# Optimization experiments

Hardware: AMD Instinct MI355X
Metric: run time of the kernel (lower is better)

The kernel has to match this reference:

```python
import jax, jax.numpy as jnp
import numpy as np

B, T, C = 8, 1024, 768
H = 12
HS = C // H  # 64


def setup_inputs() -> dict:
    key = jax.random.key(0)
    ks = jax.random.split(key, 6)
    s = C ** -0.5
    x = jax.random.normal(ks[0], (B, T, C), dtype=jnp.float32)
    Wq = jax.random.normal(ks[1], (H, C, HS), dtype=jnp.float32) * s
    Wk = jax.random.normal(ks[2], (H, C, HS), dtype=jnp.float32) * s
    Wv = jax.random.normal(ks[3], (H, C, HS), dtype=jnp.float32) * s
    Wproj = jax.random.normal(ks[4], (C, C), dtype=jnp.float32) * s
    bproj = jax.random.normal(ks[5], (C,), dtype=jnp.float32) * 0.01
    return {"x": x, "Wq": Wq, "Wk": Wk, "Wv": Wv, "Wproj": Wproj, "bproj": bproj}


def reference(x, Wq, Wk, Wv, Wproj, bproj):
    # per-head projections (equivalent to stacked per-head nn.Linear, bias=False)
    q = jnp.einsum('btc,hcd->bhtd', x, Wq)
    k = jnp.einsum('btc,hcd->bhtd', x, Wk)
    v = jnp.einsum('btc,hcd->bhtd', x, Wv)
    scale = HS ** -0.5
    scores = jnp.einsum('bhtd,bhsd->bhts', q, k) * scale  # [B,H,T,T]
    causal = jnp.tril(jnp.ones((T, T), dtype=bool))
    scores = jnp.where(causal, scores, -jnp.inf)
    weights = jax.nn.softmax(scores, axis=-1)
    out = jnp.einsum('bhts,bhsd->bhtd', weights, v)  # [B,H,T,HS]
    out = out.transpose(0, 2, 1, 3).reshape(B, T, C)  # concat heads
    # output projection (dropout is identity in eval mode)
    return out @ Wproj.T + bproj
```

## Files before the change

### kernel.cpp

```cpp
#include <hip/hip_runtime.h>
#include <hip/hip_bf16.h>


typedef short bf16x8 __attribute__((ext_vector_type(8)));
typedef float f32x4 __attribute__((ext_vector_type(4)));

static __device__ __forceinline__ unsigned short f2bf(float f) {
  unsigned int u = __float_as_uint(f);
  u += 0x7fffu + ((u >> 16) & 1u);
  return (unsigned short)(u >> 16);
}

static __device__ __forceinline__ unsigned int pk2bf(float a, float b) {
  union { __hip_bfloat162 h; unsigned int u; } c;
  c.h = __float22bfloat162_rn(make_float2(a, b));
  return c.u;
}

static __device__ __forceinline__ void gl_lds16(const void* g, void* l) {
  __builtin_amdgcn_global_load_lds(
      (const __attribute__((address_space(1))) unsigned int*)g,
      (__attribute__((address_space(3))) unsigned int*)l, 16, 0, 0);
}

__global__ __launch_bounds__(256) void k_prep(
    const float* __restrict__ x, const float* __restrict__ Wproj,
    const float* __restrict__ Wq, const float* __restrict__ Wk,
    const float* __restrict__ Wv,
    unsigned short* __restrict__ xb, unsigned short* __restrict__ wp,
    unsigned short* __restrict__ wt) {
  __shared__ float tb[64][65];
  const int bx = blockIdx.x;
  const int tid = threadIdx.x;
  if (bx < 6720) {
    const float* src = (bx < 6144) ? x : Wproj;
    unsigned short* dst = (bx < 6144) ? xb : wp;
    int i = (bx < 6144 ? bx : bx - 6144) * 256 + tid;
    float4 f = ((const float4*)src)[i];
    uint2 o;
    o.x = pk2bf(f.x, f.y);
    o.y = pk2bf(f.z, f.w);
    ((uint2*)dst)[i] = o;
    return;
  }
  const int idx = bx - 6720;
  const int c0 = (idx % 12) * 64;
  const int hq = idx / 12;
  const int qi = hq / 12, h = hq % 12;
  const float* W = (qi == 0) ? Wq : ((qi == 1) ? Wk : Wv);
  {
    int rowb = tid >> 4;
    int col4 = (tid & 15) * 4;
#pragma unroll
    for (int it = 0; it < 4; ++it) {
      int c = it * 16 + rowb;
      float4 f = *(const float4*)(W + (h * 768 + c0 + c) * 64 + col4);
      tb[c][col4] = f.x; tb[c][col4 + 1] = f.y; tb[c][col4 + 2] = f.z; tb[c][col4 + 3] = f.w;
    }
  }
  __syncthreads();
#pragma unroll
  for (int it = 0; it < 2; ++it) {
    int slot = it * 256 + tid;
    int d = slot >> 3, cg = (slot & 7) * 8;
    union { unsigned int u[4]; uint4 v; } o;
#pragma unroll
    for (int j = 0; j < 4; ++j)
      o.u[j] = pk2bf(tb[cg + 2 * j][d], tb[cg + 2 * j + 1][d]);
    *(uint4*)(wt + (qi * 768 + h * 64 + d) * 768 + c0 + cg) = o.v;
  }
}

__global__ __launch_bounds__(256) void k_gemm_qkv(
    const unsigned short* __restrict__ xb,
    const unsigned short* __restrict__ wt,
    unsigned short* __restrict__ qkv,
    unsigned short* __restrict__ vt) {
  __shared__ unsigned short As[128 * 32];
  __shared__ unsigned short Bs[128 * 32];
  const int tid = threadIdx.x;
  const int w = tid >> 6, lane = tid & 63, quad = lane >> 4, lr = lane & 15;
  const int wm = w >> 1, wn = w & 1;
  const int m0 = blockIdx.x * 128, n0 = blockIdx.y * 128;

  f32x4 acc[4][4] = {};

  const int srow = w * 16 + (lane >> 2);
  const int su = (lane & 3) ^ ((srow >> 1) & 3);
  const int scol = su * 8;
  const unsigned short* ga0 = xb + (m0 + srow) * 768 + scol;
  const unsigned short* ga1 = ga0 + 64 * 768;
  const unsigned short* gb0 = wt + (n0 + srow) * 768 + scol;
  const unsigned short* gb1 = gb0 + 64 * 768;
  unsigned short* la0 = &As[(w * 16) * 32];
  unsigned short* la1 = la0 + 64 * 32;
  unsigned short* lb0 = &Bs[(w * 16) * 32];
  unsigned short* lb1 = lb0 + 64 * 32;

  const int fu = quad ^ ((lr >> 1) & 3);

  for (int k0 = 0; k0 < 768; k0 += 32) {
    gl_lds16(ga0 + k0, la0);
    gl_lds16(ga1 + k0, la1);
    gl_lds16(gb0 + k0, lb0);
    gl_lds16(gb1 + k0, lb1);
    __syncthreads();
    bf16x8 af[4], bfr[4];
#pragma unroll
    for (int i = 0; i < 4; ++i)
      af[i] = *(const bf16x8*)(&As[(wm * 64 + i * 16 + lr) * 32 + fu * 8]);
#pragma unroll
    for (int j = 0; j < 4; ++j)
      bfr[j] = *(const bf16x8*)(&Bs[(wn * 64 + j * 16 + lr) * 32 + fu * 8]);
#pragma unroll
    for (int j = 0; j < 4; ++j)
#pragma unroll
      for (int i = 0; i < 4; ++i)
        acc[j][i] = __builtin_amdgcn_mfma_f32_16x16x32_bf16(bfr[j], af[i], acc[j][i], 0, 0, 0);
    __syncthreads();
  }

  const int b = m0 >> 10, t0 = m0 & 1023;
  if (n0 < 1536) {
    const int qi = n0 / 768;
    const int rr0 = n0 - qi * 768;
#pragma unroll
    for (int j = 0; j < 4; ++j) {
      int nn = rr0 + wn * 64 + j * 16 + quad * 4;
      int h = nn >> 6, d0 = nn & 63;
      unsigned short* hb = qkv + (size_t)((qi * 8 + b) * 12 + h) * 65536 + d0;
#pragma unroll
      for (int i = 0; i < 4; ++i) {
        int t = t0 + wm * 64 + i * 16 + lr;
        uint2 o;
        o.x = pk2bf(acc[j][i][0], acc[j][i][1]);
        o.y = pk2bf(acc[j][i][2], acc[j][i][3]);
        *(uint2*)(hb + (size_t)t * 64) = o;
      }
    }
  } else {
    const int rr0 = n0 - 1536;
#pragma unroll
    for (int j = 0; j < 4; ++j) {
      int nn = rr0 + wn * 64 + j * 16 + quad * 4;
      int h = nn >> 6, d0 = nn & 63;
      unsigned short* vrow = vt + (size_t)((b * 12 + h) * 64 + d0) * 1024;
#pragma unroll
      for (int i = 0; i < 4; ++i) {
        int t = t0 + wm * 64 + i * 16 + lr;
#pragma unroll
        for (int r = 0; r < 4; ++r)
          vrow[(size_t)r * 1024 + t] = f2bf(acc[j][i][r]);
      }
    }
  }
}

__global__ __launch_bounds__(256) void k_attn(
    const unsigned short* __restrict__ qkv,
    const unsigned short* __restrict__ Vtg,
    unsigned short* __restrict__ attn) {
  __shared__ unsigned short Kbuf[2][64 * 64];
  __shared__ unsigned short Vbuf[2][64 * 64];
  __shared__ unsigned short Pbuf[4][32 * 68];
  const int tid = threadIdx.x;
  const int w = tid >> 6, lane = tid & 63, quad = lane >> 4, lr = lane & 15;
  const int hb = blockIdx.x;
  const int qb = 7 - (int)blockIdx.y;
  const int h = hb % 12, b = hb / 12;
  const int HT = 65536;
  const unsigned short* Q  = qkv + (b * 12 + h) * HT;
  const unsigned short* K  = qkv + (96 + b * 12 + h) * HT;
  const unsigned short* Vt = Vtg + (b * 12 + h) * HT;

  bf16x8 aq[2][2];
#pragma unroll
  for (int i = 0; i < 2; ++i)
#pragma unroll
    for (int hf = 0; hf < 2; ++hf)
      aq[i][hf] = *(const bf16x8*)(Q + (qb * 128 + w * 32 + i * 16 + lr) * 64 + hf * 32 + quad * 8);

  f32x4 accO[2][4] = {};
  float lsum[2][4] = {};

  const int nc = 2 * qb + 2;
  const float c1 = 0.125f * 1.4426950408889634f;
  const float c0 = -4.0f * 1.4426950408889634f;

  auto stage = [&](int bi, int sc) {
#pragma unroll
    for (int j = 0; j < 2; ++j) {
      int row = w * 16 + j * 8 + (lane >> 3);
      int c8 = (lane & 7) ^ (row & 7);
      gl_lds16(K + (sc * 64 + row) * 64 + c8 * 8, &Kbuf[bi][(w * 16 + j * 8) * 64]);
      gl_lds16(Vt + row * 1024 + sc * 64 + c8 * 8, &Vbuf[bi][(w * 16 + j * 8) * 64]);
    }
  };

  stage(0, 0);
  for (int sc = 0; sc < nc; ++sc) {
    __syncthreads();
    if (sc + 1 < nc) stage((sc + 1) & 1, sc + 1);
    const unsigned short* Kl = Kbuf[sc & 1];
    const unsigned short* Vl = Vbuf[sc & 1];

    f32x4 accS[2][4];
#pragma unroll
    for (int i = 0; i < 2; ++i)
#pragma unroll
      for (int nt = 0; nt < 4; ++nt) {
        f32x4 z = {};
#pragma unroll
        for (int hf = 0; hf < 2; ++hf) {
          int s = nt * 16 + lr;
          bf16x8 kb = *(const bf16x8*)(Kl + (s * 8 + ((4 * hf + quad) ^ (s & 7))) * 8);
          z = __builtin_amdgcn_mfma_f32_16x16x32_bf16(aq[i][hf], kb, z, 0, 0, 0);
        }
        accS[i][nt] = z;
      }

#pragma unroll
    for (int i = 0; i < 2; ++i) {
      const int base_i = qb * 128 + w * 32 + i * 16;
      const bool needmask = (sc * 64 + 63 > base_i);
#pragma unroll
      for (int r = 0; r < 4; ++r) {
        int tg = base_i + quad * 4 + r;
        unsigned short* prow = &Pbuf[w][(i * 16 + quad * 4 + r) * 68 + lr];
        float p[4];
#pragma unroll
        for (int nt = 0; nt < 4; ++nt) {
          float e = __builtin_amdgcn_exp2f(fmaf(accS[i][nt][r], c1, c0));
          if (needmask && (sc * 64 + nt * 16 + lr > tg)) e = 0.f;
          lsum[i][r] += e;
          p[nt] = e;
        }
        unsigned int u01 = pk2bf(p[0], p[1]);
        unsigned int u23 = pk2bf(p[2], p[3]);
        prow[0]  = (unsigned short)(u01 & 0xffffu);
        prow[16] = (unsigned short)(u01 >> 16);
        prow[32] = (unsigned short)(u23 & 0xffffu);
        prow[48] = (unsigned short)(u23 >> 16);
      }
    }

#pragma unroll
    for (int i = 0; i < 2; ++i) {
      bf16x8 pa[2];
#pragma unroll
      for (int hf = 0; hf < 2; ++hf)
        pa[hf] = *(const bf16x8*)(&Pbuf[w][(i * 16 + lr) * 68 + hf * 32 + quad * 8]);
#pragma unroll
      for (int ntd = 0; ntd < 4; ++ntd) {
        int d = ntd * 16 + lr;
#pragma unroll
        for (int hf = 0; hf < 2; ++hf) {
          bf16x8 vb = *(const bf16x8*)(Vl + (d * 8 + ((4 * hf + quad) ^ (d & 7))) * 8);
          accO[i][ntd] = __builtin_amdgcn_mfma_f32_16x16x32_bf16(pa[hf], vb, accO[i][ntd], 0, 0, 0);
        }
      }
    }
  }

  float linv[2][4];
#pragma unroll
  for (int i = 0; i < 2; ++i)
#pragma unroll
    for (int r = 0; r < 4; ++r) {
      float l = lsum[i][r];
      l += __shfl_xor(l, 1);
      l += __shfl_xor(l, 2);
      l += __shfl_xor(l, 4);
      l += __shfl_xor(l, 8);
      linv[i][r] = 1.0f / l;
    }

#pragma unroll
  for (int i = 0; i < 2; ++i)
#pragma unroll
    for (int ntd = 0; ntd < 4; ++ntd) {
      int c = h * 64 + ntd * 16 + lr;
#pragma unroll
      for (int r = 0; r < 4; ++r) {
        int t = qb * 128 + w * 32 + i * 16 + quad * 4 + r;
        attn[(b * 1024 + t) * 768 + c] = f2bf(accO[i][ntd][r] * linv[i][r]);
      }
    }
}

__global__ __launch_bounds__(256) void k_gemm_proj(
    const unsigned short* __restrict__ ab,
    const unsigned short* __restrict__ wp,
    const float* __restrict__ bias,
    float* __restrict__ out) {
  __shared__ unsigned short As[128 * 32];
  __shared__ unsigned short Bs[128 * 32];
  const int tid = threadIdx.x;
  const int w = tid >> 6, lane = tid & 63, quad = lane >> 4, lr = lane & 15;
  const int wm = w >> 1, wn = w & 1;
  const int m0 = blockIdx.x * 128, n0 = blockIdx.y * 128;

  f32x4 acc[4][4] = {};

  const int srow = w * 16 + (lane >> 2);
  const int su = (lane & 3) ^ ((srow >> 1) & 3);
  const int scol = su * 8;
  const unsigned short* ga0 = ab + (m0 + srow) * 768 + scol;
  const unsigned short* ga1 = ga0 + 64 * 768;
  const unsigned short* gb0 = wp + (n0 + srow) * 768 + scol;
  const unsigned short* gb1 = gb0 + 64 * 768;
  unsigned short* la0 = &As[(w * 16) * 32];
  unsigned short* la1 = la0 + 64 * 32;
  unsigned short* lb0 = &Bs[(w * 16) * 32];
  unsigned short* lb1 = lb0 + 64 * 32;

  const int fu = quad ^ ((lr >> 1) & 3);

  for (int k0 = 0; k0 < 768; k0 += 32) {
    gl_lds16(ga0 + k0, la0);
    gl_lds16(ga1 + k0, la1);
    gl_lds16(gb0 + k0, lb0);
    gl_lds16(gb1 + k0, lb1);
    __syncthreads();
    bf16x8 af[4], bfr[4];
#pragma unroll
    for (int i = 0; i < 4; ++i)
      af[i] = *(const bf16x8*)(&As[(wm * 64 + i * 16 + lr) * 32 + fu * 8]);
#pragma unroll
    for (int j = 0; j < 4; ++j)
      bfr[j] = *(const bf16x8*)(&Bs[(wn * 64 + j * 16 + lr) * 32 + fu * 8]);
#pragma unroll
    for (int j = 0; j < 4; ++j)
#pragma unroll
      for (int i = 0; i < 4; ++i)
        acc[j][i] = __builtin_amdgcn_mfma_f32_16x16x32_bf16(bfr[j], af[i], acc[j][i], 0, 0, 0);
    __syncthreads();
  }

#pragma unroll
  for (int j = 0; j < 4; ++j) {
    int ncol = n0 + wn * 64 + j * 16 + quad * 4;
    float4 bv = *(const float4*)(bias + ncol);
#pragma unroll
    for (int i = 0; i < 4; ++i) {
      int m = m0 + wm * 64 + i * 16 + lr;
      float4 v;
      v.x = acc[j][i][0] + bv.x;
      v.y = acc[j][i][1] + bv.y;
      v.z = acc[j][i][2] + bv.z;
      v.w = acc[j][i][3] + bv.w;
      *(float4*)(out + (size_t)m * 768 + ncol) = v;
    }
  }
}

extern "C" void kernel_launch(void* const* d_in, const int* in_sizes, int n_in,
                              void* d_out, int out_size, void* d_ws, size_t ws_size,
                              hipStream_t stream) {
  const float* x     = (const float*)d_in[0];
  const float* Wq    = (const float*)d_in[1];
  const float* Wk    = (const float*)d_in[2];
  const float* Wv    = (const float*)d_in[3];
  const float* Wproj = (const float*)d_in[4];
  const float* bproj = (const float*)d_in[5];
  float* out = (float*)d_out;

  char* p = (char*)d_ws;
  unsigned short* xb   = (unsigned short*)p; p += 12582912;
  unsigned short* wt   = (unsigned short*)p; p += 3538944;
  unsigned short* wp   = (unsigned short*)p; p += 1179648;
  unsigned short* qkv  = (unsigned short*)p; p += 37748736;
  unsigned short* attn = (unsigned short*)p; p += 12582912;
  unsigned short* vt   = qkv + (size_t)192 * 65536;

  k_prep<<<7152, 256, 0, stream>>>(x, Wproj, Wq, Wk, Wv, xb, wp, wt);
  k_gemm_qkv<<<dim3(64, 18), 256, 0, stream>>>(xb, wt, qkv, vt);
  k_attn<<<dim3(96, 8), 256, 0, stream>>>(qkv, vt, attn);
  k_gemm_proj<<<dim3(64, 6), 256, 0, stream>>>(attn, wp, bproj, out);
}
```

Measured before the change: 184.3 us.

## Double-buffer LDS with 64-wide K tiles in QKV and projection GEMMs

Both bf16 GEMM kernels now stage K tiles of 64 instead of 32 into two alternating LDS buffers. The next tile's global-to-LDS load is issued right after a single barrier, so it can overlap the MFMA work on the current tile. The LDS swizzle is changed to an XOR over 8 column groups to match the wider tile. This halves the number of K iterations and barriers, at the cost of four times the LDS per block (64 KB), which may reduce how many blocks fit on a CU.

```diff
diff --git a/kernel.cpp b/kernel.cpp
--- a/kernel.cpp
+++ b/kernel.cpp
@@ -76,8 +76,8 @@
     const unsigned short* __restrict__ wt,
     unsigned short* __restrict__ qkv,
     unsigned short* __restrict__ vt) {
-  __shared__ unsigned short As[128 * 32];
-  __shared__ unsigned short Bs[128 * 32];
+  __shared__ unsigned short As[2][128 * 64];
+  __shared__ unsigned short Bs[2][128 * 64];
   const int tid = threadIdx.x;
   const int w = tid >> 6, lane = tid & 63, quad = lane >> 4, lr = lane & 15;
   const int wm = w >> 1, wn = w & 1;
@@ -85,39 +85,40 @@
 
   f32x4 acc[4][4] = {};
 
-  const int srow = w * 16 + (lane >> 2);
-  const int su = (lane & 3) ^ ((srow >> 1) & 3);
-  const int scol = su * 8;
-  const unsigned short* ga0 = xb + (m0 + srow) * 768 + scol;
-  const unsigned short* ga1 = ga0 + 64 * 768;
-  const unsigned short* gb0 = wt + (n0 + srow) * 768 + scol;
-  const unsigned short* gb1 = gb0 + 64 * 768;
-  unsigned short* la0 = &As[(w * 16) * 32];
-  unsigned short* la1 = la0 + 64 * 32;
-  unsigned short* lb0 = &Bs[(w * 16) * 32];
-  unsigned short* lb1 = lb0 + 64 * 32;
-
-  const int fu = quad ^ ((lr >> 1) & 3);
-
-  for (int k0 = 0; k0 < 768; k0 += 32) {
-    gl_lds16(ga0 + k0, la0);
-    gl_lds16(ga1 + k0, la1);
-    gl_lds16(gb0 + k0, lb0);
-    gl_lds16(gb1 + k0, lb1);
+  const int su = (lane & 7) ^ (lane >> 3);
+  const unsigned short* ga = xb + (size_t)(m0 + w * 8 + (lane >> 3)) * 768 + su * 8;
+  const unsigned short* gb = wt + (size_t)(n0 + w * 8 + (lane >> 3)) * 768 + su * 8;
+
+  auto stage = [&](int bi, int kt) {
+    const int k0 = kt * 64;
+#pragma unroll
+    for (int j = 0; j < 4; ++j) {
+      gl_lds16(ga + (size_t)j * 32 * 768 + k0, &As[bi][(j * 32 + w * 8) * 64]);
+      gl_lds16(gb + (size_t)j * 32 * 768 + k0, &Bs[bi][(j * 32 + w * 8) * 64]);
+    }
+  };
+
+  stage(0, 0);
+  for (int kt = 0; kt < 12; ++kt) {
     __syncthreads();
-    bf16x8 af[4], bfr[4];
-#pragma unroll
-    for (int i = 0; i < 4; ++i)
-      af[i] = *(const bf16x8*)(&As[(wm * 64 + i * 16 + lr) * 32 + fu * 8]);
-#pragma unroll
-    for (int j = 0; j < 4; ++j)
-      bfr[j] = *(const bf16x8*)(&Bs[(wn * 64 + j * 16 + lr) * 32 + fu * 8]);
-#pragma unroll
-    for (int j = 0; j < 4; ++j)
+    if (kt < 11) stage((kt + 1) & 1, kt + 1);
+    const unsigned short* Al = As[kt & 1];
+    const unsigned short* Bl = Bs[kt & 1];
+#pragma unroll
+    for (int hf = 0; hf < 2; ++hf) {
+      bf16x8 af[4], bfr[4];
 #pragma unroll
       for (int i = 0; i < 4; ++i)
-        acc[j][i] = __builtin_amdgcn_mfma_f32_16x16x32_bf16(bfr[j], af[i], acc[j][i], 0, 0, 0);
-    __syncthreads();
+        af[i] = *(const bf16x8*)(&Al[(wm * 64 + i * 16 + lr) * 64 + ((4 * hf + quad) ^ (lr & 7)) * 8]);
+#pragma unroll
+      for (int j = 0; j < 4; ++j)
+        bfr[j] = *(const bf16x8*)(&Bl[(wn * 64 + j * 16 + lr) * 64 + ((4 * hf + quad) ^ (lr & 7)) * 8]);
+#pragma unroll
+      for (int j = 0; j < 4; ++j)
+#pragma unroll
+        for (int i = 0; i < 4; ++i)
+          acc[j][i] = __builtin_amdgcn_mfma_f32_16x16x32_bf16(bfr[j], af[i], acc[j][i], 0, 0, 0);
+    }
   }
 
   const int b = m0 >> 10, t0 = m0 & 1023;
@@ -293,8 +294,8 @@
     const unsigned short* __restrict__ wp,
     const float* __restrict__ bias,
     float* __restrict__ out) {
-  __shared__ unsigned short As[128 * 32];
-  __shared__ unsigned short Bs[128 * 32];
+  __shared__ unsigned short As[2][128 * 64];
+  __shared__ unsigned short Bs[2][128 * 64];
   const int tid = threadIdx.x;
   const int w = tid >> 6, lane = tid & 63, quad = lane >> 4, lr = lane & 15;
   const int wm = w >> 1, wn = w & 1;
@@ -302,39 +303,40 @@
 
   f32x4 acc[4][4] = {};
 
-  const int srow = w * 16 + (lane >> 2);
-  const int su = (lane & 3) ^ ((srow >> 1) & 3);
-  const int scol = su * 8;
-  const unsigned short* ga0 = ab + (m0 + srow) * 768 + scol;
-  const unsigned short* ga1 = ga0 + 64 * 768;
-  const unsigned short* gb0 = wp + (n0 + srow) * 768 + scol;
-  const unsigned short* gb1 = gb0 + 64 * 768;
-  unsigned short* la0 = &As[(w * 16) * 32];
-  unsigned short* la1 = la0 + 64 * 32;
-  unsigned short* lb0 = &Bs[(w * 16) * 32];
-  unsigned short* lb1 = lb0 + 64 * 32;
-
-  const int fu = quad ^ ((lr >> 1) & 3);
-
-  for (int k0 = 0; k0 < 768; k0 += 32) {
-    gl_lds16(ga0 + k0, la0);
-    gl_lds16(ga1 + k0, la1);
-    gl_lds16(gb0 + k0, lb0);
-    gl_lds16(gb1 + k0, lb1);
+  const int su = (lane & 7) ^ (lane >> 3);
+  const unsigned short* ga = ab + (size_t)(m0 + w * 8 + (lane >> 3)) * 768 + su * 8;
+  const unsigned short* gb = wp + (size_t)(n0 + w * 8 + (lane >> 3)) * 768 + su * 8;
+
+  auto stage = [&](int bi, int kt) {
+    const int k0 = kt * 64;
+#pragma unroll
+    for (int j = 0; j < 4; ++j) {
+      gl_lds16(ga + (size_t)j * 32 * 768 + k0, &As[bi][(j * 32 + w * 8) * 64]);
+      gl_lds16(gb + (size_t)j * 32 * 768 + k0, &Bs[bi][(j * 32 + w * 8) * 64]);
+    }
+  };
+
+  stage(0, 0);
+  for (int kt = 0; kt < 12; ++kt) {
     __syncthreads();
-    bf16x8 af[4], bfr[4];
-#pragma unroll
-    for (int i = 0; i < 4; ++i)
-      af[i] = *(const bf16x8*)(&As[(wm * 64 + i * 16 + lr) * 32 + fu * 8]);
-#pragma unroll
-    for (int j = 0; j < 4; ++j)
-      bfr[j] = *(const bf16x8*)(&Bs[(wn * 64 + j * 16 + lr) * 32 + fu * 8]);
-#pragma unroll
-    for (int j = 0; j < 4; ++j)
+    if (kt < 11) stage((kt + 1) & 1, kt + 1);
+    const unsigned short* Al = As[kt & 1];
+    const unsigned short* Bl = Bs[kt & 1];
+#pragma unroll
+    for (int hf = 0; hf < 2; ++hf) {
+      bf16x8 af[4], bfr[4];
 #pragma unroll
       for (int i = 0; i < 4; ++i)
-        acc[j][i] = __builtin_amdgcn_mfma_f32_16x16x32_bf16(bfr[j], af[i], acc[j][i], 0, 0, 0);
-    __syncthreads();
+        af[i] = *(const bf16x8*)(&Al[(wm * 64 + i * 16 + lr) * 64 + ((4 * hf + quad) ^ (lr & 7)) * 8]);
+#pragma unroll
+      for (int j = 0; j < 4; ++j)
+        bfr[j] = *(const bf16x8*)(&Bl[(wn * 64 + j * 16 + lr) * 64 + ((4 * hf + quad) ^ (lr & 7)) * 8]);
+#pragma unroll
+      for (int j = 0; j < 4; ++j)
+#pragma unroll
+        for (int i = 0; i < 4; ++i)
+          acc[j][i] = __builtin_amdgcn_mfma_f32_16x16x32_bf16(bfr[j], af[i], acc[j][i], 0, 0, 0);
+    }
   }
 
 #pragma unroll
```

New measurement: 194.5 us. +5.5%, slower.
